# Kernel tuning notes

Measured on AMD Instinct MI355X. Metric: run time of the kernel, lower is better.

## Reference

```python
import jax, jax.numpy as jnp
import numpy as np

N = 100000   # nodes
E = 1600000  # edges
D = 128      # feature dim (layers all 128)
G = 512      # graphs in batch
C = 10       # num_classes
EPS = 1e-5   # batchnorm eps


def setup_inputs() -> dict:
    key = jax.random.key(0)
    ks = jax.random.split(key, 16)
    s = 1.0 / np.sqrt(D)
    return {
        "x": jax.random.normal(ks[0], (N, D), jnp.float32),
        "edge_index": jax.random.randint(ks[1], (2, E), 0, N),
        "batch": jnp.sort(jax.random.randint(ks[2], (N,), 0, G)),
        "w1": jax.random.normal(ks[3], (D, D), jnp.float32) * s,
        "b1": jnp.zeros((D,), jnp.float32),
        "w2": jax.random.normal(ks[4], (D, D), jnp.float32) * s,
        "b2": jnp.zeros((D,), jnp.float32),
        "w3": jax.random.normal(ks[5], (D, D), jnp.float32) * s,
        "b3": jnp.zeros((D,), jnp.float32),
        "g1": jnp.ones((D,), jnp.float32),
        "be1": jnp.zeros((D,), jnp.float32),
        "g2": jnp.ones((D,), jnp.float32),
        "be2": jnp.zeros((D,), jnp.float32),
        "fc_w": jax.random.normal(ks[6], (D, C), jnp.float32) * s,
        "fc_b": jnp.zeros((C,), jnp.float32),
    }


def _gcn(x, src, dst, norm, W, b):
    # transform -> gather -> normalize -> scatter-add (PyG GCNConv)
    h = x @ W
    out = jax.ops.segment_sum(h[src] * norm[:, None], dst, num_segments=x.shape[0])
    return out + b


def _bn(x, g, b):
    # training-mode BatchNorm1d: batch mean / biased variance
    mu = jnp.mean(x, axis=0)
    var = jnp.mean((x - mu) ** 2, axis=0)
    return (x - mu) * jax.lax.rsqrt(var + EPS) * g + b


def reference(x, edge_index, batch, w1, b1, w2, b2, w3, b3, g1, be1, g2, be2, fc_w, fc_b):
    n = x.shape[0]
    loop = jnp.arange(n)
    src = jnp.concatenate([edge_index[0], loop])  # add self-loops
    dst = jnp.concatenate([edge_index[1], loop])
    deg = jax.ops.segment_sum(jnp.ones_like(src, x.dtype), dst, num_segments=n)
    dinv = jax.lax.rsqrt(jnp.maximum(deg, 1.0))  # deg >= 1 due to self-loops
    norm = dinv[src] * dinv[dst]  # symmetric normalization per edge

    h = jax.nn.relu(_gcn(x, src, dst, norm, w1, b1))        # conv1 + relu (bn1 unused, per source)
    h = jax.nn.relu(_gcn(h, src, dst, norm, w2, b2))        # conv2 + relu
    h = jax.nn.relu(_bn(h, g1, be1))                        # bn + relu
    h = jax.nn.relu(_gcn(h, src, dst, norm, w3, b3))        # conv3 + relu
    h = jax.nn.relu(_bn(h, g2, be2))                        # bn + relu

    cnt = jax.ops.segment_sum(jnp.ones((n,), h.dtype), batch, num_segments=G)
    pooled = jax.ops.segment_sum(h, batch, num_segments=G) / jnp.maximum(cnt, 1.0)[:, None]
    logits = pooled @ fc_w + fc_b
    return jax.nn.log_softmax(logits, axis=1)
```

## Files before the change

kernel.cpp:

```cpp
#include <hip/hip_runtime.h>
#include <hip/hip_bf16.h>
#include <math.h>

#define D 128
#define G_GRAPHS 512
#define C_CLASSES 10
#define BN_EPS 1e-5f
#define NBUCK_MAX 512
#define EDGE_CHUNK 4096
#define EPT 16

typedef unsigned short u16;
typedef unsigned short ushort4_t __attribute__((ext_vector_type(4)));
typedef unsigned short ushort8_t __attribute__((ext_vector_type(8)));
typedef __bf16 bf16x8 __attribute__((ext_vector_type(8)));
typedef float floatx4 __attribute__((ext_vector_type(4)));
union B8 { ushort8_t u; bf16x8 b; };

__device__ __forceinline__ float bf_lo(unsigned int v) { return __uint_as_float(v << 16); }
__device__ __forceinline__ float bf_hi(unsigned int v) { return __uint_as_float(v & 0xffff0000u); }
__device__ __forceinline__ u16 f2bf(float f) {
    union { float f; unsigned int u; } x; x.f = f;
    unsigned int r = x.u + 0x7fff + ((x.u >> 16) & 1);
    return (u16)(r >> 16);
}


__global__ __launch_bounds__(256) void bucket_hist_kernel(
    const int* __restrict__ dst, int* __restrict__ bucketCnt, int E, int nbuck)
{
    __shared__ int h[NBUCK_MAX];
    int tid = threadIdx.x;
    for (int i = tid; i < NBUCK_MAX; i += 256) h[i] = 0;
    __syncthreads();
    for (int i = blockIdx.x * 256 + tid; i < E; i += gridDim.x * 256)
        atomicAdd(&h[dst[i] >> 8], 1);
    __syncthreads();
    for (int i = tid; i < nbuck; i += 256)
        if (h[i]) atomicAdd(&bucketCnt[i], h[i]);
}

__global__ void scan_buckets_kernel(
    const int* __restrict__ bucketCnt, int* __restrict__ bucketBase,
    int* __restrict__ bucketCursor, int* __restrict__ rowPtr, int nbuck, int N, int E)
{
    __shared__ int buf[2][512];
    int tid = threadIdx.x;
    int v = (tid < nbuck) ? bucketCnt[tid] : 0;
    buf[0][tid] = v;
    __syncthreads();
    int cur = 0;
    for (int off = 1; off < 512; off <<= 1) {
        buf[1 - cur][tid] = buf[cur][tid] + ((tid >= off) ? buf[cur][tid - off] : 0);
        cur ^= 1;
        __syncthreads();
    }
    if (tid < nbuck) {
        int b = buf[cur][tid] - v;
        bucketBase[tid] = b;
        bucketCursor[tid] = b;
    }
    if (tid == 0) { bucketBase[nbuck] = E; rowPtr[N] = E; }
}

__global__ __launch_bounds__(256) void scatter_pairs_kernel(
    const int* __restrict__ src, const int* __restrict__ dst,
    int* __restrict__ bucketCursor, uint2* __restrict__ pairs, int E)
{
    __shared__ int h[NBUCK_MAX];
    __shared__ int base[NBUCK_MAX];
    int tid = threadIdx.x;
    int e0 = blockIdx.x * EDGE_CHUNK;
    for (int i = tid; i < NBUCK_MAX; i += 256) h[i] = 0;
    __syncthreads();
    int s[EPT], d[EPT], r[EPT];
#pragma unroll
    for (int j = 0; j < EPT; ++j) {
        int i = e0 + j * 256 + tid;
        if (i < E) {
            s[j] = src[i];
            d[j] = dst[i];
            r[j] = atomicAdd(&h[d[j] >> 8], 1);
        } else {
            d[j] = -1;
        }
    }
    __syncthreads();
    for (int i = tid; i < NBUCK_MAX; i += 256)
        if (h[i]) base[i] = atomicAdd(&bucketCursor[i], h[i]);
    __syncthreads();
#pragma unroll
    for (int j = 0; j < EPT; ++j) {
        if (d[j] >= 0) {
            int b = d[j] >> 8;
            pairs[base[b] + r[j]] = make_uint2((unsigned)s[j], (unsigned)d[j]);
        }
    }
}

__global__ __launch_bounds__(256) void bucket_sort_kernel(
    const uint2* __restrict__ pairs, const int* __restrict__ bucketBase,
    int* __restrict__ colIdx, int* __restrict__ rowPtr, float* __restrict__ dinv, int N)
{
    __shared__ int h[256];
    __shared__ int cur[256];
    __shared__ int sbuf[2][256];
    int tid = threadIdx.x;
    int b = blockIdx.x;
    int s = bucketBase[b], e = bucketBase[b + 1];
    h[tid] = 0;
    __syncthreads();
    for (int i = s + tid; i < e; i += 256)
        atomicAdd(&h[pairs[i].y & 255], 1);
    __syncthreads();
    int cnt = h[tid];
    sbuf[0][tid] = cnt;
    __syncthreads();
    int c = 0;
    for (int off = 1; off < 256; off <<= 1) {
        sbuf[1 - c][tid] = sbuf[c][tid] + ((tid >= off) ? sbuf[c][tid - off] : 0);
        c ^= 1;
        __syncthreads();
    }
    int excl = sbuf[c][tid] - cnt;
    int v = b * 256 + tid;
    if (v < N) {
        rowPtr[v] = s + excl;
        dinv[v] = rsqrtf((float)(cnt + 1));
    }
    cur[tid] = s + excl;
    __syncthreads();
    for (int i = s + tid; i < e; i += 256) {
        uint2 p = pairs[i];
        int pos = atomicAdd(&cur[p.y & 255], 1);
        colIdx[pos] = (int)p.x;
    }
}

__global__ __launch_bounds__(256) void graph_bounds_kernel(
    const int* __restrict__ batch, int* __restrict__ gstart, int N)
{
    int i = blockIdx.x * 256 + threadIdx.x;
    if (i >= N) return;
    int b = batch[i];
    int prev = (i == 0) ? -1 : batch[i - 1];
    if (b != prev) {
        for (int g = prev + 1; g <= b; ++g) gstart[g] = i;
    }
    if (i == N - 1) {
        for (int g = b + 1; g <= G_GRAPHS; ++g) gstart[g] = N;
    }
}

__global__ __launch_bounds__(256) void wconv_kernel(
    const float4* __restrict__ w1, const float4* __restrict__ w2,
    const float4* __restrict__ w3, u16* __restrict__ wtAll)
{
    const float4* W = (blockIdx.x == 0) ? w1 : (blockIdx.x == 1) ? w2 : w3;
    u16* Wt = wtAll + (size_t)blockIdx.x * D * D;
    int tid = threadIdx.x;
#pragma unroll
    for (int i = 0; i < 16; ++i) {
        int idx = tid + i * 256;
        int k = idx >> 5, c4 = idx & 31;
        float4 v = W[idx];
        Wt[(4 * c4 + 0) * D + k] = f2bf(v.x);
        Wt[(4 * c4 + 1) * D + k] = f2bf(v.y);
        Wt[(4 * c4 + 2) * D + k] = f2bf(v.z);
        Wt[(4 * c4 + 3) * D + k] = f2bf(v.w);
    }
}

#define XS_STRIDE 136
__global__ __launch_bounds__(256) void gemm_mfma_kernel(
    const float4* __restrict__ X, const u16* __restrict__ Wt,
    const float* __restrict__ scale, const float* __restrict__ shift,
    u16* __restrict__ Y, int nrows)
{
    __shared__ __align__(16) u16 Xs[64 * XS_STRIDE];
    __shared__ __align__(16) u16 Ws[128 * XS_STRIDE];
    int tid = threadIdx.x;
    int row0 = blockIdx.x * 64;
    bool fuse = (scale != nullptr);

    const ushort8_t* Wv = (const ushort8_t*)Wt;
#pragma unroll
    for (int i = 0; i < 8; ++i) {
        int idx = tid + i * 256;
        int n = idx >> 4, c8 = idx & 15;
        *(ushort8_t*)&Ws[n * XS_STRIDE + c8 * 8] = Wv[idx];
    }
#pragma unroll
    for (int i = 0; i < 8; ++i) {
        int idx = tid + i * 256;
        int r = idx >> 5, c4 = idx & 31;
        int gr = row0 + r;
        float4 v = make_float4(0.f, 0.f, 0.f, 0.f);
        if (gr < nrows) v = X[(size_t)gr * 32 + c4];
        if (fuse) {
            int k = c4 * 4;
            v.x = fmaxf(v.x * scale[k] + shift[k], 0.f);
            v.y = fmaxf(v.y * scale[k + 1] + shift[k + 1], 0.f);
            v.z = fmaxf(v.z * scale[k + 2] + shift[k + 2], 0.f);
            v.w = fmaxf(v.w * scale[k + 3] + shift[k + 3], 0.f);
        }
        ushort4_t o;
        o.x = f2bf(v.x); o.y = f2bf(v.y); o.z = f2bf(v.z); o.w = f2bf(v.w);
        *(ushort4_t*)&Xs[r * XS_STRIDE + c4 * 4] = o;
    }
    __syncthreads();

    int wid = tid >> 6, lane = tid & 63;
    int m = lane & 15, quad = lane >> 4;
    int arow = wid * 16 + m;

    floatx4 acc[8] = {};
#pragma unroll
    for (int ks = 0; ks < 4; ++ks) {
        int kk = ks * 32 + quad * 8;
        B8 a;
        a.u = *(const ushort8_t*)&Xs[arow * XS_STRIDE + kk];
#pragma unroll
        for (int t = 0; t < 8; ++t) {
            B8 b;
            b.u = *(const ushort8_t*)&Ws[(t * 16 + m) * XS_STRIDE + kk];
            acc[t] = __builtin_amdgcn_mfma_f32_16x16x32_bf16(a.b, b.b, acc[t], 0, 0, 0);
        }
    }

#pragma unroll
    for (int t = 0; t < 8; ++t) {
#pragma unroll
        for (int r = 0; r < 4; ++r) {
            int grow = row0 + wid * 16 + quad * 4 + r;
            if (grow < nrows) Y[(size_t)grow * D + t * 16 + m] = f2bf(acc[t][r]);
        }
    }
}

__global__ __launch_bounds__(256) void aggregate_kernel(
    const uint4* __restrict__ T, const int* __restrict__ colIdx,
    const int* __restrict__ rowPtr, const float* __restrict__ dinv,
    const float* __restrict__ bias, float* __restrict__ outH, int n)
{
    int wid = threadIdx.x >> 6;
    int lane = threadIdx.x & 63;
    int row = blockIdx.x * 4 + wid;
    if (row >= n) return;
    int fg = lane & 15;
    int eg = lane >> 4;

    float dr = dinv[row];
    float acc[8] = {};

    if (eg == 0) {
        uint4 sv = T[(size_t)row * 16 + fg];
        acc[0] = dr * bf_lo(sv.x); acc[1] = dr * bf_hi(sv.x);
        acc[2] = dr * bf_lo(sv.y); acc[3] = dr * bf_hi(sv.y);
        acc[4] = dr * bf_lo(sv.z); acc[5] = dr * bf_hi(sv.z);
        acc[6] = dr * bf_lo(sv.w); acc[7] = dr * bf_hi(sv.w);
    }

    int s = rowPtr[row], e = rowPtr[row + 1];
    for (int j0 = s; j0 < e; j0 += 64) {
        int m = e - j0;
        if (m > 64) m = 64;
        int u = row;
        float du = 0.f;
        if (lane < m) {
            u = colIdx[j0 + lane];
            du = dinv[u];
        }
        int nt = (m + 3) >> 2;
        for (int t = 0; t < nt; ++t) {
            int idx = t * 4 + eg;
            int uu = __shfl(u, idx);
            float duu = __shfl(du, idx);
            uint4 tw = T[(size_t)uu * 16 + fg];
            acc[0] += duu * bf_lo(tw.x); acc[1] += duu * bf_hi(tw.x);
            acc[2] += duu * bf_lo(tw.y); acc[3] += duu * bf_hi(tw.y);
            acc[4] += duu * bf_lo(tw.z); acc[5] += duu * bf_hi(tw.z);
            acc[6] += duu * bf_lo(tw.w); acc[7] += duu * bf_hi(tw.w);
        }
    }

#pragma unroll
    for (int off = 16; off < 64; off <<= 1) {
#pragma unroll
        for (int i = 0; i < 8; ++i) acc[i] += __shfl_xor(acc[i], off);
    }

    const float2* bp = (const float2*)bias;
    int pidx = fg * 4 + eg;
    float2 b = bp[pidx];
    float2 o;
    o.x = fmaxf(dr * acc[eg * 2] + b.x, 0.f);
    o.y = fmaxf(dr * acc[eg * 2 + 1] + b.y, 0.f);
    ((float2*)outH)[(size_t)row * 64 + pidx] = o;
}

__global__ __launch_bounds__(256) void bn_stats_kernel(
    const float* __restrict__ H, int n, float* __restrict__ gsum, float* __restrict__ gsq)
{
    int tid = threadIdx.x;
    int col = tid & 127;
    float s = 0.f, s2 = 0.f;
    for (int row = blockIdx.x * 2 + (tid >> 7); row < n; row += gridDim.x * 2) {
        float v = H[(size_t)row * D + col];
        s += v;
        s2 += v * v;
    }
    __shared__ float sh[256], sh2[256];
    sh[tid] = s;
    sh2[tid] = s2;
    __syncthreads();
    if (tid < 128) {
        atomicAdd(&gsum[col], sh[tid] + sh[tid + 128]);
        atomicAdd(&gsq[col], sh2[tid] + sh2[tid + 128]);
    }
}

__global__ void bn_finalize_kernel(const float* __restrict__ gsum, const float* __restrict__ gsq,
                                   const float* __restrict__ gamma, const float* __restrict__ beta,
                                   float n, float* __restrict__ scale, float* __restrict__ shift)
{
    int c = threadIdx.x;
    float mu = gsum[c] / n;
    float var = gsq[c] / n - mu * mu;
    float sc = gamma[c] * rsqrtf(var + BN_EPS);
    scale[c] = sc;
    shift[c] = beta[c] - mu * sc;
}

__global__ __launch_bounds__(128) void pool_kernel(
    const float* __restrict__ H, const float* __restrict__ scale, const float* __restrict__ shift,
    const int* __restrict__ gstart, float* __restrict__ pooled)
{
    int g = blockIdx.x;
    int tid = threadIdx.x;
    int s = gstart[g], c = gstart[g + 1] - s;
    float sc = scale[tid], sh = shift[tid];
    float a = 0.f;
    for (int i = 0; i < c; ++i) {
        float v = H[(size_t)(s + i) * D + tid];
        a += fmaxf(v * sc + sh, 0.f);
    }
    int cm = c > 1 ? c : 1;
    pooled[(size_t)g * D + tid] = a / (float)cm;
}

__global__ __launch_bounds__(64) void classify_kernel(
    const float* __restrict__ pooled, const float* __restrict__ fcw,
    const float* __restrict__ fcb, float* __restrict__ out)
{
    int g = blockIdx.x;
    int tid = threadIdx.x;
    __shared__ float prow[D];
    __shared__ float lg[C_CLASSES];
    prow[tid] = pooled[(size_t)g * D + tid];
    prow[tid + 64] = pooled[(size_t)g * D + 64 + tid];
    __syncthreads();
    if (tid < C_CLASSES) {
        float s = fcb[tid];
        for (int d = 0; d < D; ++d) s += prow[d] * fcw[d * C_CLASSES + tid];
        lg[tid] = s;
    }
    __syncthreads();
    if (tid == 0) {
        float m = -1e30f;
        for (int c = 0; c < C_CLASSES; ++c) m = fmaxf(m, lg[c]);
        float se = 0.f;
        for (int c = 0; c < C_CLASSES; ++c) se += expf(lg[c] - m);
        float lse = m + logf(se);
        for (int c = 0; c < C_CLASSES; ++c) out[(size_t)g * C_CLASSES + c] = lg[c] - lse;
    }
}

extern "C" void kernel_launch(void* const* d_in, const int* in_sizes, int n_in,
                              void* d_out, int out_size, void* d_ws, size_t ws_size,
                              hipStream_t stream) {
    const float* x   = (const float*)d_in[0];
    const int* ei    = (const int*)d_in[1];
    const int* batch = (const int*)d_in[2];
    const float* w1  = (const float*)d_in[3];
    const float* b1  = (const float*)d_in[4];
    const float* w2  = (const float*)d_in[5];
    const float* b2  = (const float*)d_in[6];
    const float* w3  = (const float*)d_in[7];
    const float* b3  = (const float*)d_in[8];
    const float* g1  = (const float*)d_in[9];
    const float* be1 = (const float*)d_in[10];
    const float* g2  = (const float*)d_in[11];
    const float* be2 = (const float*)d_in[12];
    const float* fcw = (const float*)d_in[13];
    const float* fcb = (const float*)d_in[14];

    const int N = in_sizes[0] / D;
    const int E = in_sizes[1] / 2;
    const int* src = ei;
    const int* dst = ei + E;
    const int nbuck = (N + 255) >> 8;

    char* p = (char*)d_ws;
    auto alloc = [&](size_t bytes) -> void* {
        void* r = (void*)p;
        p += (bytes + 255) & ~(size_t)255;
        return r;
    };
    float* dinv     = (float*)alloc((size_t)N * 4);
    int*   rowPtr   = (int*)alloc((size_t)(N + 1) * 4);
    int*   colIdx   = (int*)alloc((size_t)E * 4);
    uint2* pairs    = (uint2*)alloc((size_t)E * 8);
    int*   bucketCnt    = (int*)alloc(NBUCK_MAX * 4);
    int*   bucketBase   = (int*)alloc((NBUCK_MAX + 1) * 4);
    int*   bucketCursor = (int*)alloc(NBUCK_MAX * 4);
    int*   gstart  = (int*)alloc((G_GRAPHS + 1) * 4);
    float* statsacc= (float*)alloc(4 * D * 4);
    float* gsum1 = statsacc, *gsq1 = statsacc + D, *gsum2 = statsacc + 2 * D, *gsq2 = statsacc + 3 * D;
    float* sc1     = (float*)alloc(D * 4);
    float* sh1     = (float*)alloc(D * 4);
    float* sc2     = (float*)alloc(D * 4);
    float* sh2     = (float*)alloc(D * 4);
    float* pooled  = (float*)alloc((size_t)G_GRAPHS * D * 4);
    u16*   wtAll   = (u16*)alloc((size_t)3 * D * D * 2);
    u16*   tmp     = (u16*)alloc((size_t)N * D * 2);
    float* hbuf    = (float*)alloc((size_t)N * D * 4);

    hipMemsetAsync(bucketCnt, 0, NBUCK_MAX * 4, stream);
    hipMemsetAsync(statsacc, 0, 4 * D * 4, stream);

    bucket_hist_kernel<<<512, 256, 0, stream>>>(dst, bucketCnt, E, nbuck);
    scan_buckets_kernel<<<1, 512, 0, stream>>>(bucketCnt, bucketBase, bucketCursor, rowPtr, nbuck, N, E);
    scatter_pairs_kernel<<<(E + EDGE_CHUNK - 1) / EDGE_CHUNK, 256, 0, stream>>>(src, dst, bucketCursor, pairs, E);
    bucket_sort_kernel<<<nbuck, 256, 0, stream>>>(pairs, bucketBase, colIdx, rowPtr, dinv, N);
    graph_bounds_kernel<<<(N + 255) / 256, 256, 0, stream>>>(batch, gstart, N);
    wconv_kernel<<<3, 256, 0, stream>>>((const float4*)w1, (const float4*)w2, (const float4*)w3, wtAll);

    const int GB = (N + 63) / 64;
    const int AB = (N + 3) / 4;

    gemm_mfma_kernel<<<GB, 256, 0, stream>>>((const float4*)x, wtAll, nullptr, nullptr, tmp, N);
    aggregate_kernel<<<AB, 256, 0, stream>>>((const uint4*)tmp, colIdx, rowPtr, dinv, b1, hbuf, N);
    gemm_mfma_kernel<<<GB, 256, 0, stream>>>((const float4*)hbuf, wtAll + D * D, nullptr, nullptr, tmp, N);
    aggregate_kernel<<<AB, 256, 0, stream>>>((const uint4*)tmp, colIdx, rowPtr, dinv, b2, hbuf, N);
    bn_stats_kernel<<<512, 256, 0, stream>>>(hbuf, N, gsum1, gsq1);
    bn_finalize_kernel<<<1, 128, 0, stream>>>(gsum1, gsq1, g1, be1, (float)N, sc1, sh1);
    gemm_mfma_kernel<<<GB, 256, 0, stream>>>((const float4*)hbuf, wtAll + 2 * D * D, sc1, sh1, tmp, N);
    aggregate_kernel<<<AB, 256, 0, stream>>>((const uint4*)tmp, colIdx, rowPtr, dinv, b3, hbuf, N);
    bn_stats_kernel<<<512, 256, 0, stream>>>(hbuf, N, gsum2, gsq2);
    bn_finalize_kernel<<<1, 128, 0, stream>>>(gsum2, gsq2, g2, be2, (float)N, sc2, sh2);
    pool_kernel<<<G_GRAPHS, 128, 0, stream>>>(hbuf, sc2, sh2, gstart, pooled);
    classify_kernel<<<G_GRAPHS, 64, 0, stream>>>(pooled, fcw, fcb, (float*)d_out);
}
```

Before: 600.7 us.

## Store hidden activations in bf16, pack edge pairs, vectorize GEMM output stores

```diff
diff --git a/kernel.cpp b/kernel.cpp
--- a/kernel.cpp
+++ b/kernel.cpp
@@ -11,18 +11,22 @@
 #define EPT 16
 
 typedef unsigned short u16;
+typedef unsigned int u32;
 typedef unsigned short ushort4_t __attribute__((ext_vector_type(4)));
 typedef unsigned short ushort8_t __attribute__((ext_vector_type(8)));
 typedef __bf16 bf16x8 __attribute__((ext_vector_type(8)));
 typedef float floatx4 __attribute__((ext_vector_type(4)));
 union B8 { ushort8_t u; bf16x8 b; };
 
-__device__ __forceinline__ float bf_lo(unsigned int v) { return __uint_as_float(v << 16); }
-__device__ __forceinline__ float bf_hi(unsigned int v) { return __uint_as_float(v & 0xffff0000u); }
+__device__ __forceinline__ float bf_lo(u32 v) { return __uint_as_float(v << 16); }
+__device__ __forceinline__ float bf_hi(u32 v) { return __uint_as_float(v & 0xffff0000u); }
 __device__ __forceinline__ u16 f2bf(float f) {
-    union { float f; unsigned int u; } x; x.f = f;
-    unsigned int r = x.u + 0x7fff + ((x.u >> 16) & 1);
+    union { float f; u32 u; } x; x.f = f;
+    u32 r = x.u + 0x7fff + ((x.u >> 16) & 1);
     return (u16)(r >> 16);
+}
+__device__ __forceinline__ u32 pack2bf(float a, float b) {
+    return (u32)f2bf(a) | ((u32)f2bf(b) << 16);
 }
 
 
@@ -65,7 +69,7 @@
 
 __global__ __launch_bounds__(256) void scatter_pairs_kernel(
     const int* __restrict__ src, const int* __restrict__ dst,
-    int* __restrict__ bucketCursor, uint2* __restrict__ pairs, int E)
+    int* __restrict__ bucketCursor, u32* __restrict__ pairs, int E)
 {
     __shared__ int h[NBUCK_MAX];
     __shared__ int base[NBUCK_MAX];
@@ -93,13 +97,13 @@
     for (int j = 0; j < EPT; ++j) {
         if (d[j] >= 0) {
             int b = d[j] >> 8;
-            pairs[base[b] + r[j]] = make_uint2((unsigned)s[j], (unsigned)d[j]);
+            pairs[base[b] + r[j]] = ((u32)s[j] << 8) | (u32)(d[j] & 255);
         }
     }
 }
 
 __global__ __launch_bounds__(256) void bucket_sort_kernel(
-    const uint2* __restrict__ pairs, const int* __restrict__ bucketBase,
+    const u32* __restrict__ pairs, const int* __restrict__ bucketBase,
     int* __restrict__ colIdx, int* __restrict__ rowPtr, float* __restrict__ dinv, int N)
 {
     __shared__ int h[256];
@@ -111,7 +115,7 @@
     h[tid] = 0;
     __syncthreads();
     for (int i = s + tid; i < e; i += 256)
-        atomicAdd(&h[pairs[i].y & 255], 1);
+        atomicAdd(&h[pairs[i] & 255], 1);
     __syncthreads();
     int cnt = h[tid];
     sbuf[0][tid] = cnt;
@@ -131,9 +135,9 @@
     cur[tid] = s + excl;
     __syncthreads();
     for (int i = s + tid; i < e; i += 256) {
-        uint2 p = pairs[i];
-        int pos = atomicAdd(&cur[p.y & 255], 1);
-        colIdx[pos] = (int)p.x;
+        u32 p = pairs[i];
+        int pos = atomicAdd(&cur[p & 255], 1);
+        colIdx[pos] = (int)(p >> 8);
     }
 }
 
@@ -172,17 +176,40 @@
 }
 
 #define XS_STRIDE 136
-__global__ __launch_bounds__(256) void gemm_mfma_kernel(
-    const float4* __restrict__ X, const u16* __restrict__ Wt,
-    const float* __restrict__ scale, const float* __restrict__ shift,
-    u16* __restrict__ Y, int nrows)
-{
-    __shared__ __align__(16) u16 Xs[64 * XS_STRIDE];
-    __shared__ __align__(16) u16 Ws[128 * XS_STRIDE];
-    int tid = threadIdx.x;
-    int row0 = blockIdx.x * 64;
-    bool fuse = (scale != nullptr);
-
+
+__device__ __forceinline__ void gemm_core_and_store(
+    const u16* Xs, const u16* Ws, u16* __restrict__ Y, int row0, int nrows, int tid)
+{
+    int wid = tid >> 6, lane = tid & 63;
+    int m = lane & 15, quad = lane >> 4;
+    int xrow = wid * 16 + m;
+
+    floatx4 acc[8] = {};
+#pragma unroll
+    for (int ks = 0; ks < 4; ++ks) {
+        int kk = ks * 32 + quad * 8;
+        B8 a;
+        a.u = *(const ushort8_t*)&Xs[xrow * XS_STRIDE + kk];
+#pragma unroll
+        for (int t = 0; t < 8; ++t) {
+            B8 b;
+            b.u = *(const ushort8_t*)&Ws[(t * 16 + m) * XS_STRIDE + kk];
+            acc[t] = __builtin_amdgcn_mfma_f32_16x16x32_bf16(b.b, a.b, acc[t], 0, 0, 0);
+        }
+    }
+    int grow = row0 + xrow;
+    if (grow < nrows) {
+#pragma unroll
+        for (int t = 0; t < 8; ++t) {
+            ushort4_t o;
+            o.x = f2bf(acc[t][0]); o.y = f2bf(acc[t][1]);
+            o.z = f2bf(acc[t][2]); o.w = f2bf(acc[t][3]);
+            *(ushort4_t*)&Y[(size_t)grow * D + t * 16 + quad * 4] = o;
+        }
+    }
+}
+
+__device__ __forceinline__ void stage_w(const u16* __restrict__ Wt, u16* Ws, int tid) {
     const ushort8_t* Wv = (const ushort8_t*)Wt;
 #pragma unroll
     for (int i = 0; i < 8; ++i) {
@@ -190,6 +217,17 @@
         int n = idx >> 4, c8 = idx & 15;
         *(ushort8_t*)&Ws[n * XS_STRIDE + c8 * 8] = Wv[idx];
     }
+}
+
+__global__ __launch_bounds__(256) void gemm_mfma_f32in_kernel(
+    const float4* __restrict__ X, const u16* __restrict__ Wt,
+    u16* __restrict__ Y, int nrows)
+{
+    __shared__ __align__(16) u16 Xs[64 * XS_STRIDE];
+    __shared__ __align__(16) u16 Ws[128 * XS_STRIDE];
+    int tid = threadIdx.x;
+    int row0 = blockIdx.x * 64;
+    stage_w(Wt, Ws, tid);
 #pragma unroll
     for (int i = 0; i < 8; ++i) {
         int idx = tid + i * 256;
@@ -197,51 +235,53 @@
         int gr = row0 + r;
         float4 v = make_float4(0.f, 0.f, 0.f, 0.f);
         if (gr < nrows) v = X[(size_t)gr * 32 + c4];
-        if (fuse) {
-            int k = c4 * 4;
-            v.x = fmaxf(v.x * scale[k] + shift[k], 0.f);
-            v.y = fmaxf(v.y * scale[k + 1] + shift[k + 1], 0.f);
-            v.z = fmaxf(v.z * scale[k + 2] + shift[k + 2], 0.f);
-            v.w = fmaxf(v.w * scale[k + 3] + shift[k + 3], 0.f);
-        }
         ushort4_t o;
         o.x = f2bf(v.x); o.y = f2bf(v.y); o.z = f2bf(v.z); o.w = f2bf(v.w);
         *(ushort4_t*)&Xs[r * XS_STRIDE + c4 * 4] = o;
     }
     __syncthreads();
-
-    int wid = tid >> 6, lane = tid & 63;
-    int m = lane & 15, quad = lane >> 4;
-    int arow = wid * 16 + m;
-
-    floatx4 acc[8] = {};
-#pragma unroll
-    for (int ks = 0; ks < 4; ++ks) {
-        int kk = ks * 32 + quad * 8;
-        B8 a;
-        a.u = *(const ushort8_t*)&Xs[arow * XS_STRIDE + kk];
-#pragma unroll
-        for (int t = 0; t < 8; ++t) {
-            B8 b;
-            b.u = *(const ushort8_t*)&Ws[(t * 16 + m) * XS_STRIDE + kk];
-            acc[t] = __builtin_amdgcn_mfma_f32_16x16x32_bf16(a.b, b.b, acc[t], 0, 0, 0);
-        }
-    }
-
-#pragma unroll
-    for (int t = 0; t < 8; ++t) {
-#pragma unroll
-        for (int r = 0; r < 4; ++r) {
-            int grow = row0 + wid * 16 + quad * 4 + r;
-            if (grow < nrows) Y[(size_t)grow * D + t * 16 + m] = f2bf(acc[t][r]);
-        }
-    }
+    gemm_core_and_store(Xs, Ws, Y, row0, nrows, tid);
+}
+
+__global__ __launch_bounds__(256) void gemm_mfma_bf16in_kernel(
+    const uint4* __restrict__ X, const u16* __restrict__ Wt,
+    const float* __restrict__ scale, const float* __restrict__ shift,
+    u16* __restrict__ Y, int nrows)
+{
+    __shared__ __align__(16) u16 Xs[64 * XS_STRIDE];
+    __shared__ __align__(16) u16 Ws[128 * XS_STRIDE];
+    int tid = threadIdx.x;
+    int row0 = blockIdx.x * 64;
+    bool fuse = (scale != nullptr);
+    stage_w(Wt, Ws, tid);
+#pragma unroll
+    for (int i = 0; i < 4; ++i) {
+        int idx = tid + i * 256;
+        int r = idx >> 4, c8 = idx & 15;
+        int gr = row0 + r;
+        uint4 v = make_uint4(0, 0, 0, 0);
+        if (gr < nrows) v = X[(size_t)gr * 16 + c8];
+        if (fuse) {
+            int k = c8 * 8;
+            v.x = pack2bf(fmaxf(bf_lo(v.x) * scale[k]     + shift[k],     0.f),
+                          fmaxf(bf_hi(v.x) * scale[k + 1] + shift[k + 1], 0.f));
+            v.y = pack2bf(fmaxf(bf_lo(v.y) * scale[k + 2] + shift[k + 2], 0.f),
+                          fmaxf(bf_hi(v.y) * scale[k + 3] + shift[k + 3], 0.f));
+            v.z = pack2bf(fmaxf(bf_lo(v.z) * scale[k + 4] + shift[k + 4], 0.f),
+                          fmaxf(bf_hi(v.z) * scale[k + 5] + shift[k + 5], 0.f));
+            v.w = pack2bf(fmaxf(bf_lo(v.w) * scale[k + 6] + shift[k + 6], 0.f),
+                          fmaxf(bf_hi(v.w) * scale[k + 7] + shift[k + 7], 0.f));
+        }
+        *(uint4*)&Xs[r * XS_STRIDE + c8 * 8] = v;
+    }
+    __syncthreads();
+    gemm_core_and_store(Xs, Ws, Y, row0, nrows, tid);
 }
 
 __global__ __launch_bounds__(256) void aggregate_kernel(
     const uint4* __restrict__ T, const int* __restrict__ colIdx,
     const int* __restrict__ rowPtr, const float* __restrict__ dinv,
-    const float* __restrict__ bias, float* __restrict__ outH, int n)
+    const float* __restrict__ bias, u32* __restrict__ outH, int n)
 {
     int wid = threadIdx.x >> 6;
     int lane = threadIdx.x & 63;
@@ -293,30 +333,34 @@
     const float2* bp = (const float2*)bias;
     int pidx = fg * 4 + eg;
     float2 b = bp[pidx];
-    float2 o;
-    o.x = fmaxf(dr * acc[eg * 2] + b.x, 0.f);
-    o.y = fmaxf(dr * acc[eg * 2 + 1] + b.y, 0.f);
-    ((float2*)outH)[(size_t)row * 64 + pidx] = o;
+    float ox = fmaxf(dr * acc[eg * 2] + b.x, 0.f);
+    float oy = fmaxf(dr * acc[eg * 2 + 1] + b.y, 0.f);
+    outH[(size_t)row * 64 + pidx] = pack2bf(ox, oy);
 }
 
 __global__ __launch_bounds__(256) void bn_stats_kernel(
-    const float* __restrict__ H, int n, float* __restrict__ gsum, float* __restrict__ gsq)
-{
-    int tid = threadIdx.x;
-    int col = tid & 127;
-    float s = 0.f, s2 = 0.f;
-    for (int row = blockIdx.x * 2 + (tid >> 7); row < n; row += gridDim.x * 2) {
-        float v = H[(size_t)row * D + col];
-        s += v;
-        s2 += v * v;
-    }
-    __shared__ float sh[256], sh2[256];
-    sh[tid] = s;
-    sh2[tid] = s2;
-    __syncthreads();
-    if (tid < 128) {
-        atomicAdd(&gsum[col], sh[tid] + sh[tid + 128]);
-        atomicAdd(&gsq[col], sh2[tid] + sh2[tid + 128]);
+    const u32* __restrict__ H, int n, float* __restrict__ gsum, float* __restrict__ gsq)
+{
+    int tid = threadIdx.x;
+    int c = tid & 63, rr = tid >> 6;
+    float sA = 0.f, sA2 = 0.f, sB = 0.f, sB2 = 0.f;
+    for (int row = blockIdx.x * 4 + rr; row < n; row += gridDim.x * 4) {
+        u32 v = H[(size_t)row * 64 + c];
+        float a = bf_lo(v), b = bf_hi(v);
+        sA += a; sA2 += a * a; sB += b; sB2 += b * b;
+    }
+    __shared__ float shA[256], shA2[256], shB[256], shB2[256];
+    shA[tid] = sA; shA2[tid] = sA2; shB[tid] = sB; shB2[tid] = sB2;
+    __syncthreads();
+    if (tid < 64) {
+        float tA = shA[tid] + shA[tid + 64] + shA[tid + 128] + shA[tid + 192];
+        float tA2 = shA2[tid] + shA2[tid + 64] + shA2[tid + 128] + shA2[tid + 192];
+        float tB = shB[tid] + shB[tid + 64] + shB[tid + 128] + shB[tid + 192];
+        float tB2 = shB2[tid] + shB2[tid + 64] + shB2[tid + 128] + shB2[tid + 192];
+        atomicAdd(&gsum[2 * c], tA);
+        atomicAdd(&gsq[2 * c], tA2);
+        atomicAdd(&gsum[2 * c + 1], tB);
+        atomicAdd(&gsq[2 * c + 1], tB2);
     }
 }
 
@@ -332,21 +376,31 @@
     shift[c] = beta[c] - mu * sc;
 }
 
-__global__ __launch_bounds__(128) void pool_kernel(
-    const float* __restrict__ H, const float* __restrict__ scale, const float* __restrict__ shift,
+__global__ __launch_bounds__(256) void pool_kernel(
+    const u32* __restrict__ H, const float* __restrict__ scale, const float* __restrict__ shift,
     const int* __restrict__ gstart, float* __restrict__ pooled)
 {
     int g = blockIdx.x;
     int tid = threadIdx.x;
-    int s = gstart[g], c = gstart[g + 1] - s;
-    float sc = scale[tid], sh = shift[tid];
-    float a = 0.f;
-    for (int i = 0; i < c; ++i) {
-        float v = H[(size_t)(s + i) * D + tid];
-        a += fmaxf(v * sc + sh, 0.f);
-    }
-    int cm = c > 1 ? c : 1;
-    pooled[(size_t)g * D + tid] = a / (float)cm;
+    int c = tid & 63, q = tid >> 6;
+    int s = gstart[g], cnt = gstart[g + 1] - s;
+    float scA = scale[2 * c], shA = shift[2 * c];
+    float scB = scale[2 * c + 1], shB = shift[2 * c + 1];
+    float aA = 0.f, aB = 0.f;
+    for (int i = q; i < cnt; i += 4) {
+        u32 v = H[(size_t)(s + i) * 64 + c];
+        aA += fmaxf(bf_lo(v) * scA + shA, 0.f);
+        aB += fmaxf(bf_hi(v) * scB + shB, 0.f);
+    }
+    __shared__ float shAa[256], shBb[256];
+    shAa[tid] = aA; shBb[tid] = aB;
+    __syncthreads();
+    if (tid < 64) {
+        float tA = shAa[tid] + shAa[tid + 64] + shAa[tid + 128] + shAa[tid + 192];
+        float tB = shBb[tid] + shBb[tid + 64] + shBb[tid + 128] + shBb[tid + 192];
+        float inv = 1.f / (float)(cnt > 1 ? cnt : 1);
+        ((float2*)pooled)[(size_t)g * 64 + c] = make_float2(tA * inv, tB * inv);
+    }
 }
 
 __global__ __launch_bounds__(64) void classify_kernel(
@@ -410,7 +464,7 @@
     float* dinv     = (float*)alloc((size_t)N * 4);
     int*   rowPtr   = (int*)alloc((size_t)(N + 1) * 4);
     int*   colIdx   = (int*)alloc((size_t)E * 4);
-    uint2* pairs    = (uint2*)alloc((size_t)E * 8);
+    u32*   pairs    = (u32*)alloc((size_t)E * 4);
     int*   bucketCnt    = (int*)alloc(NBUCK_MAX * 4);
     int*   bucketBase   = (int*)alloc((NBUCK_MAX + 1) * 4);
     int*   bucketCursor = (int*)alloc(NBUCK_MAX * 4);
@@ -424,7 +478,7 @@
     float* pooled  = (float*)alloc((size_t)G_GRAPHS * D * 4);
     u16*   wtAll   = (u16*)alloc((size_t)3 * D * D * 2);
     u16*   tmp     = (u16*)alloc((size_t)N * D * 2);
-    float* hbuf    = (float*)alloc((size_t)N * D * 4);
+    u16*   hbuf    = (u16*)alloc((size_t)N * D * 2);
 
     hipMemsetAsync(bucketCnt, 0, NBUCK_MAX * 4, stream);
     hipMemsetAsync(statsacc, 0, 4 * D * 4, stream);
@@ -439,16 +493,16 @@
     const int GB = (N + 63) / 64;
     const int AB = (N + 3) / 4;
 
-    gemm_mfma_kernel<<<GB, 256, 0, stream>>>((const float4*)x, wtAll, nullptr, nullptr, tmp, N);
-    aggregate_kernel<<<AB, 256, 0, stream>>>((const uint4*)tmp, colIdx, rowPtr, dinv, b1, hbuf, N);
-    gemm_mfma_kernel<<<GB, 256, 0, stream>>>((const float4*)hbuf, wtAll + D * D, nullptr, nullptr, tmp, N);
-    aggregate_kernel<<<AB, 256, 0, stream>>>((const uint4*)tmp, colIdx, rowPtr, dinv, b2, hbuf, N);
-    bn_stats_kernel<<<512, 256, 0, stream>>>(hbuf, N, gsum1, gsq1);
+    gemm_mfma_f32in_kernel<<<GB, 256, 0, stream>>>((const float4*)x, wtAll, tmp, N);
+    aggregate_kernel<<<AB, 256, 0, stream>>>((const uint4*)tmp, colIdx, rowPtr, dinv, b1, (u32*)hbuf, N);
+    gemm_mfma_bf16in_kernel<<<GB, 256, 0, stream>>>((const uint4*)hbuf, wtAll + D * D, nullptr, nullptr, tmp, N);
+    aggregate_kernel<<<AB, 256, 0, stream>>>((const uint4*)tmp, colIdx, rowPtr, dinv, b2, (u32*)hbuf, N);
+    bn_stats_kernel<<<256, 256, 0, stream>>>((const u32*)hbuf, N, gsum1, gsq1);
     bn_finalize_kernel<<<1, 128, 0, stream>>>(gsum1, gsq1, g1, be1, (float)N, sc1, sh1);
-    gemm_mfma_kernel<<<GB, 256, 0, stream>>>((const float4*)hbuf, wtAll + 2 * D * D, sc1, sh1, tmp, N);
-    aggregate_kernel<<<AB, 256, 0, stream>>>((const uint4*)tmp, colIdx, rowPtr, dinv, b3, hbuf, N);
-    bn_stats_kernel<<<512, 256, 0, stream>>>(hbuf, N, gsum2, gsq2);
+    gemm_mfma_bf16in_kernel<<<GB, 256, 0, stream>>>((const uint4*)hbuf, wtAll + 2 * D * D, sc1, sh1, tmp, N);
+    aggregate_kernel<<<AB, 256, 0, stream>>>((const uint4*)tmp, colIdx, rowPtr, dinv, b3, (u32*)hbuf, N);
+    bn_stats_kernel<<<256, 256, 0, stream>>>((const u32*)hbuf, N, gsum2, gsq2);
     bn_finalize_kernel<<<1, 128, 0, stream>>>(gsum2, gsq2, g2, be2, (float)N, sc2, sh2);
-    pool_kernel<<<G_GRAPHS, 128, 0, stream>>>(hbuf, sc2, sh2, gstart, pooled);
+    pool_kernel<<<G_GRAPHS, 256, 0, stream>>>((const u32*)hbuf, sc2, sh2, gstart, pooled);
     classify_kernel<<<G_GRAPHS, 64, 0, stream>>>(pooled, fcw, fcb, (float*)d_out);
 }
```

After: 539.6 us. 1.11x faster.
